# Optimization experiments

Hardware: AMD Instinct MI355X
Metric: run time of the kernel (lower is better)

Reference implementation:

```python
import jax, jax.numpy as jnp
import numpy as np

N_NODES = 50000
N_EDGES = 320000
B = 4096          # subgraph batch: users/items/subg nodes
IN_N = 64         # in_nfeats
IN_E = 16         # in_efeats
OUT_E = 2 * IN_E  # out_edge_feats = in_efeats*2
H = 4             # num_heads
D = 64            # latent dim per layer (latent_dim=[64,64])
L = 2             # num EGAT layers


def setup_inputs() -> dict:
    key = jax.random.key(0)
    ks = iter(jax.random.split(key, 48))
    def nrm(shape, s=0.05):
        return jax.random.normal(next(ks), shape, dtype=jnp.float32) * s
    inp = {}
    inp['x'] = jax.random.normal(next(ks), (N_NODES, IN_N), dtype=jnp.float32)
    inp['efeat'] = jax.random.normal(next(ks), (N_EDGES, IN_E), dtype=jnp.float32)
    inp['efeat2'] = jax.random.normal(next(ks), (N_EDGES, IN_N), dtype=jnp.float32)
    inp['edge_mask'] = (jax.random.uniform(next(ks), (N_EDGES,)) > 0.1).astype(jnp.float32)
    inp['edge_mask2'] = (jax.random.uniform(next(ks), (N_EDGES,)) > 0.1).astype(jnp.float32)
    inp['src'] = jax.random.randint(next(ks), (N_EDGES,), 0, N_NODES, dtype=jnp.int32)
    inp['dst'] = jax.random.randint(next(ks), (N_EDGES,), 0, N_NODES, dtype=jnp.int32)
    inp['user_idx'] = jnp.arange(0, B, dtype=jnp.int32)          # ntype==0
    inp['item_idx'] = jnp.arange(B, 2 * B, dtype=jnp.int32)      # ntype==1
    inp['subg_idx'] = jnp.arange(2 * B, 3 * B, dtype=jnp.int32)  # ntype==-1
    # stacked per-layer EGAT params (layer dims identical since IN_N == D)
    inp['loc_wni'] = nrm((L, D, H * OUT_E))
    inp['loc_wnj'] = nrm((L, D, H * OUT_E))
    inp['loc_we'] = nrm((L, IN_E, H * OUT_E))
    inp['loc_attn'] = nrm((L, H, OUT_E))
    inp['loc_wnode'] = nrm((L, D, H * D))
    inp['agg1_w'] = nrm((L, H * D, D))
    inp['agg1_b'] = jnp.zeros((L, D), jnp.float32)
    inp['glob_wni'] = nrm((L, D, H * OUT_E))
    inp['glob_wnj'] = nrm((L, D, H * OUT_E))
    inp['glob_we'] = nrm((L, IN_N, H * OUT_E))
    inp['glob_attn'] = nrm((L, H, OUT_E))
    inp['glob_wnode'] = nrm((L, D, H * D))
    inp['agg2_w'] = nrm((L, H * D, D))
    inp['agg2_b'] = jnp.zeros((L, D), jnp.float32)
    inp['w1_ui'] = nrm((2 * L * D, 128))
    inp['b1_ui'] = jnp.zeros((128,), jnp.float32)
    inp['w1_sg'] = nrm((L * D, 128))
    inp['b1_sg'] = jnp.zeros((128,), jnp.float32)
    inp['w2_ui'] = nrm((128, 1))
    inp['b2_ui'] = jnp.zeros((1,), jnp.float32)
    inp['w2_sg'] = nrm((128, 1))
    inp['b2_sg'] = jnp.zeros((1,), jnp.float32)
    return inp


def _egat(x, e, norm, src, dst, wni, wnj, we, attn, wnode):
    # edge feature: f_ij = LeakyReLU(W_ni x_i + W_nj x_j + W_e e_ij), slope 0.2 (DGL EGATConv)
    f = (x @ wni)[src] + (x @ wnj)[dst] + e @ we            # (E, H*OUT_E)
    f = jax.nn.leaky_relu(f.reshape(-1, H, OUT_E), 0.2)
    scores = jnp.einsum('ehd,hd->eh', f, attn)              # (E, H)
    # edge softmax over incoming edges of each dst node
    m = jax.ops.segment_max(scores, dst, num_segments=N_NODES)
    m = jnp.where(jnp.isfinite(m), m, 0.0)
    ex = jnp.exp(scores - m[dst])
    denom = jax.ops.segment_sum(ex, dst, num_segments=N_NODES)
    a = ex / (denom[dst] + 1e-9)
    a = a * norm[:, None]                                    # per-edge norm (edge mask) weighting
    fn = (x @ wnode).reshape(-1, H, D)                       # (N, H, D)
    msg = fn[src] * a[:, :, None]                            # (E, H, D)
    out = jax.ops.segment_sum(msg, dst, num_segments=N_NODES)
    return out, a


def reference(x, efeat, efeat2, edge_mask, edge_mask2, src, dst, user_idx, item_idx, subg_idx,
              loc_wni, loc_wnj, loc_we, loc_attn, loc_wnode, agg1_w, agg1_b,
              glob_wni, glob_wnj, glob_we, glob_attn, glob_wnode, agg2_w, agg2_b,
              w1_ui, b1_ui, w1_sg, b1_sg, w2_ui, b2_ui, w2_sg, b2_sg):
    h = x
    ui_states, sg_states = [], []
    for l in range(L):
        out, _ = _egat(h, efeat, edge_mask, src, dst,
                       loc_wni[l], loc_wnj[l], loc_we[l], loc_attn[l], loc_wnode[l])
        h = jax.nn.elu(out.reshape(N_NODES, H * D) @ agg1_w[l] + agg1_b[l])
        ui_states.append(h)
        out, _ = _egat(h, efeat2, edge_mask2, src, dst,
                       glob_wni[l], glob_wnj[l], glob_we[l], glob_attn[l], glob_wnode[l])
        h = jax.nn.leaky_relu(out.reshape(N_NODES, H * D) @ agg2_w[l] + agg2_b[l], 0.01)
        sg_states.append(h)
    ui = jnp.concatenate(ui_states, axis=1)   # (N, L*D)
    sg = jnp.concatenate(sg_states, axis=1)   # (N, L*D)
    ui_x = jnp.concatenate([ui[user_idx], ui[item_idx]], axis=1)  # (B, 2*L*D)
    sg_x = sg[subg_idx]                                           # (B, L*D)
    ui_h = jax.nn.relu(ui_x @ w1_ui + b1_ui)  # dropout is identity in eval
    sg_h = jax.nn.relu(sg_x @ w1_sg + b1_sg)
    ui_out = jax.nn.sigmoid(ui_h @ w2_ui + b2_ui)[:, 0]
    sg_out = jax.nn.sigmoid(sg_h @ w2_sg + b2_sg)[:, 0]
    return (sg_out, ui_out)
```

## Files before the change

kernel.cpp:

```cpp
#include <hip/hip_runtime.h>
#include <math.h>

#define NN 50000
#define NE 320000
#define BATCH 4096

typedef __bf16 bf16x8 __attribute__((ext_vector_type(8)));
typedef float floatx4 __attribute__((ext_vector_type(4)));
typedef unsigned short ushort;
typedef unsigned int uint;

__device__ __forceinline__ float lrelu02(float x) { return x > 0.f ? x : 0.2f * x; }
__device__ __forceinline__ float b2f(ushort h) { return __uint_as_float(((uint)h) << 16); }
__device__ __forceinline__ float b2f_lo(uint u) { return __uint_as_float(u << 16); }
__device__ __forceinline__ float b2f_hi(uint u) { return __uint_as_float(u & 0xffff0000u); }
__device__ __forceinline__ ushort f2b(float x) {
    uint u = __float_as_uint(x);
    return (ushort)((u + 0x7fffu + ((u >> 16) & 1u)) >> 16);
}

template <int GLOB>
__global__ __launch_bounds__(256) void score_frag(
    const float* __restrict__ ef,
    const ushort* __restrict__ Bfrag,
    const ushort* __restrict__ hb,
    const int* __restrict__ eidx, const int* __restrict__ srcv,
    const int* __restrict__ dstv,
    const float* __restrict__ attn, float* __restrict__ scv)
{
    constexpr int KTOT = GLOB ? 192 : 160;
    constexpr int NR = KTOT / 32;
    constexpr int EFR = GLOB ? 2 : 1;
    constexpr int LDA = GLOB ? 64 : 16;
    __shared__ __align__(16) ushort As[128 * KTOT];
    const int tid = threadIdx.x;
    const int w = tid >> 6, lane = tid & 63;
    const int quad = lane >> 4, l16 = lane & 15;
    const int row = (blockIdx.x << 6) + 16 * w + l16;

    const int e_o = eidx[row];
    const int s_n = srcv[row];
    const int d_n = dstv[row];

    bf16x8 bfr[NR];
#pragma unroll
    for (int rnd = 0; rnd < EFR; rnd++) {
        uint4 av = make_uint4(0u, 0u, 0u, 0u);
        int k0 = rnd * 32 + quad * 8;
        if (GLOB || quad < 2) {
            const float* ap = ef + (size_t)e_o * LDA + k0;
            float4 f0 = *(const float4*)ap;
            float4 f1 = *(const float4*)(ap + 4);
            av.x = (uint)f2b(f0.x) | ((uint)f2b(f0.y) << 16);
            av.y = (uint)f2b(f0.z) | ((uint)f2b(f0.w) << 16);
            av.z = (uint)f2b(f1.x) | ((uint)f2b(f1.y) << 16);
            av.w = (uint)f2b(f1.z) | ((uint)f2b(f1.w) << 16);
        }
        *(uint4*)&bfr[rnd] = av;
    }
#pragma unroll
    for (int rr = 0; rr < 2; rr++)
        bfr[EFR + rr] = *(const bf16x8*)(hb + (size_t)s_n * 64 + rr * 32 + quad * 8);
#pragma unroll
    for (int rr = 0; rr < 2; rr++)
        bfr[EFR + 2 + rr] = *(const bf16x8*)(hb + (size_t)d_n * 64 + rr * 32 + quad * 8);

    for (int i = tid; i < 128 * KTOT / 8; i += 256)
        *(uint4*)(As + (size_t)i * 8) = *(const uint4*)(Bfrag + (size_t)i * 8);
    __syncthreads();

    floatx4 acc[8];
#pragma unroll
    for (int c = 0; c < 8; c++)
#pragma unroll
        for (int r = 0; r < 4; r++) acc[c][r] = 0.f;

#pragma unroll
    for (int rnd = 0; rnd < NR; rnd++) {
#pragma unroll
        for (int c = 0; c < 8; c++) {
            bf16x8 afr = *(const bf16x8*)(As + ((size_t)(c * NR + rnd) * 64 + lane) * 8);
            acc[c] = __builtin_amdgcn_mfma_f32_16x16x32_bf16(afr, bfr[rnd], acc[c], 0, 0, 0);
        }
    }

    float ph[4] = {0.f, 0.f, 0.f, 0.f};
#pragma unroll
    for (int c = 0; c < 8; c++) {
        int fbase = 16 * c + quad * 4;
        float4 at4 = *(const float4*)(attn + fbase);
        float v = lrelu02(acc[c][0]) * at4.x;
        v = fmaf(lrelu02(acc[c][1]), at4.y, v);
        v = fmaf(lrelu02(acc[c][2]), at4.z, v);
        v = fmaf(lrelu02(acc[c][3]), at4.w, v);
        ph[fbase >> 5] += v;
    }
#pragma unroll
    for (int h = 0; h < 4; h++) {
        ph[h] += __shfl_xor(ph[h], 16);
        ph[h] += __shfl_xor(ph[h], 32);
    }
    if (quad == 0)
        *(float4*)(scv + (size_t)row * 4) = make_float4(ph[0], ph[1], ph[2], ph[3]);
}

__global__ __launch_bounds__(256) void gemm_agg(
    const ushort* __restrict__ A, int M,
    const ushort* __restrict__ Bt,
    const float* __restrict__ bias, int act,
    ushort* __restrict__ outb)
{
    __shared__ __align__(16) ushort As[64 * 32];
    __shared__ __align__(16) ushort Bs[64 * 32];
    const int tid = threadIdx.x;
    const int row0 = blockIdx.x << 6;
    const int w = tid >> 6, lane = tid & 63;
    const int quad = lane >> 4, l16 = lane & 15;
    const int arow = tid >> 2, c0 = (tid & 3) << 3;
    const int agrow = row0 + arow;

    floatx4 acc[4];
#pragma unroll
    for (int c = 0; c < 4; c++)
#pragma unroll
        for (int r = 0; r < 4; r++) acc[c][r] = 0.f;

    for (int kt = 0; kt < 256; kt += 32) {
        uint4 av = make_uint4(0u, 0u, 0u, 0u);
        if (agrow < M)
            av = *(const uint4*)(A + (size_t)agrow * 256 + kt + c0);
        *(uint4*)(As + arow * 32 + c0) = av;
        {
            int bn = tid >> 2, bk = (tid & 3) << 3;
            *(uint4*)(Bs + bn * 32 + bk) = *(const uint4*)(Bt + (size_t)bn * 256 + kt + bk);
        }
        __syncthreads();
        bf16x8 af = *(const bf16x8*)(As + (16 * w + l16) * 32 + quad * 8);
#pragma unroll
        for (int c = 0; c < 4; c++) {
            bf16x8 bfv = *(const bf16x8*)(Bs + (16 * c + l16) * 32 + quad * 8);
            acc[c] = __builtin_amdgcn_mfma_f32_16x16x32_bf16(af, bfv, acc[c], 0, 0, 0);
        }
        if (kt + 32 < 256) __syncthreads();
    }
#pragma unroll
    for (int r = 0; r < 4; r++) {
        int gr = row0 + 16 * w + quad * 4 + r;
        if (gr < M) {
#pragma unroll
            for (int c = 0; c < 4; c++) {
                int col = 16 * c + l16;
                float v = acc[c][r] + bias[col];
                if (act == 0) v = v > 0.f ? v : (__expf(v) - 1.f);
                else          v = v > 0.f ? v : 0.01f * v;
                outb[(size_t)gr * 64 + col] = f2b(v);
            }
        }
    }
}

__global__ void k_count(const int* __restrict__ dst, int* __restrict__ deg, int E)
{
    for (int i = blockIdx.x * blockDim.x + threadIdx.x; i < E; i += gridDim.x * blockDim.x)
        atomicAdd(&deg[dst[i]], 1);
}

__global__ __launch_bounds__(256) void scan_local(
    const int* __restrict__ deg, int* __restrict__ rowptr, int* __restrict__ partials, int N)
{
    __shared__ int sd[256];
    int tid = threadIdx.x;
    int i = blockIdx.x * 256 + tid;
    int v = (i < N) ? deg[i] : 0;
    sd[tid] = v; __syncthreads();
#pragma unroll
    for (int off = 1; off < 256; off <<= 1) {
        int t = (tid >= off) ? sd[tid - off] : 0;
        __syncthreads();
        sd[tid] += t;
        __syncthreads();
    }
    if (i < N) rowptr[i] = sd[tid] - v;
    if (tid == 255) partials[blockIdx.x] = sd[255];
}

__global__ __launch_bounds__(256) void scan_partials(int* __restrict__ partials, int nb)
{
    __shared__ int sd[256];
    int tid = threadIdx.x;
    int v = (tid < nb) ? partials[tid] : 0;
    sd[tid] = v; __syncthreads();
#pragma unroll
    for (int off = 1; off < 256; off <<= 1) {
        int t = (tid >= off) ? sd[tid - off] : 0;
        __syncthreads();
        sd[tid] += t;
        __syncthreads();
    }
    if (tid < nb) partials[tid] = sd[tid] - v;
}

__global__ void scan_add(int* __restrict__ rowptr, const int* __restrict__ partials, int N, int E)
{
    int i = blockIdx.x * 256 + threadIdx.x;
    if (i < N) rowptr[i] += partials[i >> 8];
    if (i == 0) rowptr[N] = E;
}

__global__ void k_scatter(const int* __restrict__ dst, const int* __restrict__ rowptr,
                          int* __restrict__ cnt, int* __restrict__ eidx, int E)
{
    for (int i = blockIdx.x * blockDim.x + threadIdx.x; i < E; i += gridDim.x * blockDim.x) {
        int d = dst[i];
        int p = rowptr[d] + atomicAdd(&cnt[d], 1);
        eidx[p] = i;
    }
}

__global__ void k_sort_buckets(const int* __restrict__ rowptr, int* __restrict__ eidx, int N)
{
    int n = blockIdx.x * blockDim.x + threadIdx.x;
    if (n >= N) return;
    int beg = rowptr[n], end = rowptr[n + 1];
    for (int i = beg + 1; i < end; i++) {
        int v = eidx[i];
        int j = i - 1;
        while (j >= beg && eidx[j] > v) { eidx[j + 1] = eidx[j]; j--; }
        eidx[j + 1] = v;
    }
}

__global__ void k_emit_perm(const int* __restrict__ eidx, const int* __restrict__ src,
                            const int* __restrict__ dst,
                            const float* __restrict__ m1, const float* __restrict__ m2,
                            int* __restrict__ srcp, int* __restrict__ dstp,
                            float* __restrict__ m1p, float* __restrict__ m2p, int E)
{
    int p = blockIdx.x * blockDim.x + threadIdx.x;
    if (p < E) {
        int e = eidx[p];
        srcp[p] = src[e];
        dstp[p] = dst[e];
        m1p[p] = m1[e];
        m2p[p] = m2[e];
    }
}

__global__ void k_cvt(const float* __restrict__ in, ushort* __restrict__ out, int n)
{
    for (int i = blockIdx.x * blockDim.x + threadIdx.x; i < n; i += gridDim.x * blockDim.x)
        out[i] = f2b(in[i]);
}

__global__ void k_prep_score_all(const float* __restrict__ loc_we, const float* __restrict__ glob_we,
                                 const float* __restrict__ loc_wni, const float* __restrict__ glob_wni,
                                 const float* __restrict__ loc_wnj, const float* __restrict__ glob_wnj,
                                 ushort* __restrict__ B)
{
    int idx = blockIdx.x * 256 + threadIdx.x;
    if (idx >= 4 * 24576) return;
    int e = idx / 24576, rem = idx % 24576;
    int layer = e >> 1, gl = e & 1;
    int KTOT = gl ? 192 : 160;
    int NR = KTOT / 32;
    int ef_end = gl ? 64 : 32;
    int ef_real = gl ? 64 : 16;
    if (rem >= 128 * KTOT) return;
    int j = rem & 7, lane = (rem >> 3) & 63, t = rem >> 9;
    int c = t / NR, rnd = t % NR;
    int m = 16 * c + (lane & 15);
    int k = 32 * rnd + (lane >> 4) * 8 + j;
    const float* we  = (gl ? glob_we  + layer * 64 * 128 : loc_we  + layer * 16 * 128);
    const float* wni = (gl ? glob_wni : loc_wni) + layer * 64 * 128;
    const float* wnj = (gl ? glob_wnj : loc_wnj) + layer * 64 * 128;
    float v;
    if (k < ef_end)            v = (k < ef_real) ? we[k * 128 + m] : 0.f;
    else if (k < ef_end + 64)  v = wni[(k - ef_end) * 128 + m];
    else                       v = wnj[(k - ef_end - 64) * 128 + m];
    B[e * 24576 + rem] = f2b(v);
}

__global__ void k_fold_all(const float* __restrict__ loc_wnode, const float* __restrict__ agg1_w,
                           const float* __restrict__ glob_wnode, const float* __restrict__ agg2_w,
                           ushort* __restrict__ B)
{
    int e = blockIdx.x >> 6;
    int idx = (blockIdx.x & 63) * 256 + threadIdx.x;
    int layer = e >> 1, gl = e & 1;
    const float* wnode = (gl ? glob_wnode : loc_wnode) + layer * 64 * 256;
    const float* aggw  = (gl ? agg2_w : agg1_w) + layer * 256 * 64;
    int j = idx >> 8, col = idx & 255;
    int h = col >> 6, ii = col & 63;
    float s = 0.f;
#pragma unroll 8
    for (int k = 0; k < 64; k++)
        s = fmaf(wnode[ii * 256 + h * 64 + k], aggw[(h * 64 + k) * 64 + j], s);
    B[e * 16384 + j * 256 + col] = f2b(s);
}

__global__ __launch_bounds__(256) void node_fused(
    const float* __restrict__ scv,
    const int* __restrict__ rowptr, const int* __restrict__ srcp,
    const float* __restrict__ maskp,
    const ushort* __restrict__ hsrc,
    ushort* __restrict__ zb)
{
    int tid = threadIdx.x;
    int n = (blockIdx.x << 4) | (tid >> 4);
    int sl = tid & 15;
    int beg = rowptr[n], end = rowptr[n + 1];
    float l0 = 0.f, l1 = 0.f, l2 = 0.f, l3 = 0.f;
    float acc[4][4] = {};
#pragma unroll 2
    for (int i = beg; i < end; i++) {
        float4 s4 = *(const float4*)(scv + (size_t)i * 4);
        float mk = maskp[i];
        int s = srcp[i];
        uint2 hvv = *(const uint2*)(hsrc + (size_t)s * 64 + sl * 4);
        float t0 = __expf(s4.x), t1 = __expf(s4.y), t2 = __expf(s4.z), t3 = __expf(s4.w);
        l0 += t0; l1 += t1; l2 += t2; l3 += t3;
        float a0 = t0 * mk, a1 = t1 * mk, a2 = t2 * mk, a3 = t3 * mk;
        float hv[4] = { b2f_lo(hvv.x), b2f_hi(hvv.x), b2f_lo(hvv.y), b2f_hi(hvv.y) };
#pragma unroll
        for (int c = 0; c < 4; c++) {
            acc[0][c] = fmaf(a0, hv[c], acc[0][c]);
            acc[1][c] = fmaf(a1, hv[c], acc[1][c]);
            acc[2][c] = fmaf(a2, hv[c], acc[2][c]);
            acc[3][c] = fmaf(a3, hv[c], acc[3][c]);
        }
    }
    float inv[4] = { 1.f / (l0 + 1e-9f), 1.f / (l1 + 1e-9f),
                     1.f / (l2 + 1e-9f), 1.f / (l3 + 1e-9f) };
#pragma unroll
    for (int h = 0; h < 4; h++) {
        uint2 o;
        o.x = (uint)f2b(acc[h][0] * inv[h]) | ((uint)f2b(acc[h][1] * inv[h]) << 16);
        o.y = (uint)f2b(acc[h][2] * inv[h]) | ((uint)f2b(acc[h][3] * inv[h]) << 16);
        *(uint2*)(zb + (size_t)n * 256 + h * 64 + sl * 4) = o;
    }
}

__global__ __launch_bounds__(256) void final_ui(
    const ushort* __restrict__ s0, const ushort* __restrict__ s1,
    const int* __restrict__ uidx, const int* __restrict__ iidx,
    const float* __restrict__ w1, const float* __restrict__ b1,
    const float* __restrict__ w2, const float* __restrict__ b2, float* __restrict__ out)
{
    __shared__ float xs[4][256];
    int tid = threadIdx.x, wid = tid >> 6, lane = tid & 63;
    int r = (blockIdx.x << 2) + wid;
    int u = uidx[r], it = iidx[r];
    xs[wid][lane]       = b2f(s0[(size_t)u * 64 + lane]);
    xs[wid][64 + lane]  = b2f(s1[(size_t)u * 64 + lane]);
    xs[wid][128 + lane] = b2f(s0[(size_t)it * 64 + lane]);
    xs[wid][192 + lane] = b2f(s1[(size_t)it * 64 + lane]);
    __syncthreads();
    int c = lane << 1;
    float a0 = b1[c], a1 = b1[c + 1];
    for (int k = 0; k < 256; k++) {
        float xv = xs[wid][k];
        float2 wv = *(const float2*)(w1 + (size_t)k * 128 + c);
        a0 = fmaf(xv, wv.x, a0);
        a1 = fmaf(xv, wv.y, a1);
    }
    a0 = fmaxf(a0, 0.f);
    a1 = fmaxf(a1, 0.f);
    float2 w2v = *(const float2*)(w2 + c);
    float p = a0 * w2v.x + a1 * w2v.y;
#pragma unroll
    for (int mm = 1; mm < 64; mm <<= 1) p += __shfl_xor(p, mm);
    if (lane == 0) out[r] = 1.f / (1.f + __expf(-(p + b2[0])));
}

__global__ __launch_bounds__(256) void final_sg(
    const ushort* __restrict__ s0, const ushort* __restrict__ s1,
    const int* __restrict__ gidx,
    const float* __restrict__ w1, const float* __restrict__ b1,
    const float* __restrict__ w2, const float* __restrict__ b2, float* __restrict__ out)
{
    __shared__ float xs[4][128];
    int tid = threadIdx.x, wid = tid >> 6, lane = tid & 63;
    int r = (blockIdx.x << 2) + wid;
    int n = gidx[r];
    xs[wid][lane]      = b2f(s0[(size_t)n * 64 + lane]);
    xs[wid][64 + lane] = b2f(s1[(size_t)n * 64 + lane]);
    __syncthreads();
    int c = lane << 1;
    float a0 = b1[c], a1 = b1[c + 1];
    for (int k = 0; k < 128; k++) {
        float xv = xs[wid][k];
        float2 wv = *(const float2*)(w1 + (size_t)k * 128 + c);
        a0 = fmaf(xv, wv.x, a0);
        a1 = fmaf(xv, wv.y, a1);
    }
    a0 = fmaxf(a0, 0.f);
    a1 = fmaxf(a1, 0.f);
    float2 w2v = *(const float2*)(w2 + c);
    float p = a0 * w2v.x + a1 * w2v.y;
#pragma unroll
    for (int mm = 1; mm < 64; mm <<= 1) p += __shfl_xor(p, mm);
    if (lane == 0) out[r] = 1.f / (1.f + __expf(-(p + b2[0])));
}

extern "C" void kernel_launch(void* const* d_in, const int* in_sizes, int n_in,
                              void* d_out, int out_size, void* d_ws, size_t ws_size,
                              hipStream_t stream)
{
    const float* x       = (const float*)d_in[0];
    const float* efeat   = (const float*)d_in[1];
    const float* efeat2  = (const float*)d_in[2];
    const float* mask1   = (const float*)d_in[3];
    const float* mask2   = (const float*)d_in[4];
    const int*   src     = (const int*)d_in[5];
    const int*   dst     = (const int*)d_in[6];
    const int*   uidx    = (const int*)d_in[7];
    const int*   iidx    = (const int*)d_in[8];
    const int*   gidx    = (const int*)d_in[9];
    const float* loc_wni = (const float*)d_in[10];
    const float* loc_wnj = (const float*)d_in[11];
    const float* loc_we  = (const float*)d_in[12];
    const float* loc_attn= (const float*)d_in[13];
    const float* loc_wnode=(const float*)d_in[14];
    const float* agg1_w  = (const float*)d_in[15];
    const float* agg1_b  = (const float*)d_in[16];
    const float* glob_wni= (const float*)d_in[17];
    const float* glob_wnj= (const float*)d_in[18];
    const float* glob_we = (const float*)d_in[19];
    const float* glob_attn=(const float*)d_in[20];
    const float* glob_wnode=(const float*)d_in[21];
    const float* agg2_w  = (const float*)d_in[22];
    const float* agg2_b  = (const float*)d_in[23];
    const float* w1_ui   = (const float*)d_in[24];
    const float* b1_ui   = (const float*)d_in[25];
    const float* w1_sg   = (const float*)d_in[26];
    const float* b1_sg   = (const float*)d_in[27];
    const float* w2_ui   = (const float*)d_in[28];
    const float* b2_ui   = (const float*)d_in[29];
    const float* w2_sg   = (const float*)d_in[30];
    const float* b2_sg   = (const float*)d_in[31];

    char* wsp = (char*)d_ws;
    auto carve = [&](size_t bytes) { char* p = wsp; wsp += (bytes + 255) & ~(size_t)255; return p; };
    ushort* zb    = (ushort*)carve((size_t)NN * 256 * 2);
    ushort* hb[5];
    for (int i = 0; i < 5; i++) hb[i] = (ushort*)carve((size_t)NN * 64 * 2);
    float*  scv   = (float*)carve((size_t)NE * 16);
    float*  m1p   = (float*)carve((size_t)NE * 4);
    float*  m2p   = (float*)carve((size_t)NE * 4);
    int*    srcp  = (int*)carve((size_t)NE * 4);
    int*    dstp  = (int*)carve((size_t)NE * 4);
    int*    eidx  = (int*)carve((size_t)NE * 4);
    ushort* Bsc   = (ushort*)carve(4 * 24576 * 2);
    ushort* Bfold = (ushort*)carve(4 * 16384 * 2);
    int* deg      = (int*)carve(NN * 4);
    int* rowptr   = (int*)carve((NN + 4) * 4);
    int* partials = (int*)carve(256 * 4);

    k_prep_score_all<<<384, 256, 0, stream>>>(loc_we, glob_we, loc_wni, glob_wni,
                                              loc_wnj, glob_wnj, Bsc);
    k_fold_all<<<256, 256, 0, stream>>>(loc_wnode, agg1_w, glob_wnode, agg2_w, Bfold);
    hipMemsetAsync(deg, 0, NN * sizeof(int), stream);
    k_count<<<1280, 256, 0, stream>>>(dst, deg, NE);
    scan_local<<<196, 256, 0, stream>>>(deg, rowptr, partials, NN);
    scan_partials<<<1, 256, 0, stream>>>(partials, 196);
    scan_add<<<196, 256, 0, stream>>>(rowptr, partials, NN, NE);
    hipMemsetAsync(deg, 0, NN * sizeof(int), stream);
    k_scatter<<<1280, 256, 0, stream>>>(dst, rowptr, deg, eidx, NE);
    k_sort_buckets<<<196, 256, 0, stream>>>(rowptr, eidx, NN);
    k_emit_perm<<<1250, 256, 0, stream>>>(eidx, src, dst, mask1, mask2,
                                          srcp, dstp, m1p, m2p, NE);
    k_cvt<<<3200, 256, 0, stream>>>(x, hb[0], NN * 64);

    auto egat = [&](const ushort* hin, int e, const float* maskp, const float* attn,
                    const float* aggb, int act, ushort* hout) {
        int is_glob = e & 1;
        if (is_glob)
            score_frag<1><<<5000, 256, 0, stream>>>(efeat2, Bsc + e * 24576, hin,
                                                    eidx, srcp, dstp, attn, scv);
        else
            score_frag<0><<<5000, 256, 0, stream>>>(efeat, Bsc + e * 24576, hin,
                                                    eidx, srcp, dstp, attn, scv);
        node_fused<<<NN / 16, 256, 0, stream>>>(scv, rowptr, srcp, maskp, hin, zb);
        gemm_agg<<<782, 256, 0, stream>>>(zb, NN, Bfold + e * 16384, aggb, act, hout);
    };

    egat(hb[0], 0, m1p, loc_attn,        agg1_b,      0, hb[1]);
    egat(hb[1], 1, m2p, glob_attn,       agg2_b,      1, hb[2]);
    egat(hb[2], 2, m1p, loc_attn + 128,  agg1_b + 64, 0, hb[3]);
    egat(hb[3], 3, m2p, glob_attn + 128, agg2_b + 64, 1, hb[4]);

    float* out = (float*)d_out;
    final_sg<<<BATCH / 4, 256, 0, stream>>>(hb[2], hb[4], gidx, w1_sg, b1_sg, w2_sg, b2_sg, out);
    final_ui<<<BATCH / 4, 256, 0, stream>>>(hb[1], hb[3], uidx, iidx, w1_ui, b1_ui, w2_ui, b2_ui, out + BATCH);
}
```

Before: 598.9 us.

## Pre-permute edge features to bf16 and make score kernel persistent with prefetch

```diff
diff --git a/kernel.cpp b/kernel.cpp
--- a/kernel.cpp
+++ b/kernel.cpp
@@ -18,90 +18,109 @@
     uint u = __float_as_uint(x);
     return (ushort)((u + 0x7fffu + ((u >> 16) & 1u)) >> 16);
 }
+__device__ __forceinline__ uint pk2(float a, float b) {
+    return (uint)f2b(a) | ((uint)f2b(b) << 16);
+}
 
 template <int GLOB>
-__global__ __launch_bounds__(256) void score_frag(
-    const float* __restrict__ ef,
+__global__ __launch_bounds__(256, 3) void score_frag(
+    const ushort* __restrict__ efp,
     const ushort* __restrict__ Bfrag,
     const ushort* __restrict__ hb,
-    const int* __restrict__ eidx, const int* __restrict__ srcv,
-    const int* __restrict__ dstv,
+    const int* __restrict__ srcv, const int* __restrict__ dstv,
     const float* __restrict__ attn, float* __restrict__ scv)
 {
     constexpr int KTOT = GLOB ? 192 : 160;
     constexpr int NR = KTOT / 32;
     constexpr int EFR = GLOB ? 2 : 1;
-    constexpr int LDA = GLOB ? 64 : 16;
     __shared__ __align__(16) ushort As[128 * KTOT];
     const int tid = threadIdx.x;
     const int w = tid >> 6, lane = tid & 63;
     const int quad = lane >> 4, l16 = lane & 15;
-    const int row = (blockIdx.x << 6) + 16 * w + l16;
-
-    const int e_o = eidx[row];
-    const int s_n = srcv[row];
-    const int d_n = dstv[row];
-
-    bf16x8 bfr[NR];
-#pragma unroll
-    for (int rnd = 0; rnd < EFR; rnd++) {
-        uint4 av = make_uint4(0u, 0u, 0u, 0u);
-        int k0 = rnd * 32 + quad * 8;
-        if (GLOB || quad < 2) {
-            const float* ap = ef + (size_t)e_o * LDA + k0;
-            float4 f0 = *(const float4*)ap;
-            float4 f1 = *(const float4*)(ap + 4);
-            av.x = (uint)f2b(f0.x) | ((uint)f2b(f0.y) << 16);
-            av.y = (uint)f2b(f0.z) | ((uint)f2b(f0.w) << 16);
-            av.z = (uint)f2b(f1.x) | ((uint)f2b(f1.y) << 16);
-            av.w = (uint)f2b(f1.z) | ((uint)f2b(f1.w) << 16);
-        }
-        *(uint4*)&bfr[rnd] = av;
-    }
-#pragma unroll
-    for (int rr = 0; rr < 2; rr++)
-        bfr[EFR + rr] = *(const bf16x8*)(hb + (size_t)s_n * 64 + rr * 32 + quad * 8);
-#pragma unroll
-    for (int rr = 0; rr < 2; rr++)
-        bfr[EFR + 2 + rr] = *(const bf16x8*)(hb + (size_t)d_n * 64 + rr * 32 + quad * 8);
 
     for (int i = tid; i < 128 * KTOT / 8; i += 256)
         *(uint4*)(As + (size_t)i * 8) = *(const uint4*)(Bfrag + (size_t)i * 8);
+
+    auto loadB = [&](bf16x8* dstf, int r, int s, int d) {
+        if (GLOB) {
+#pragma unroll
+            for (int rr = 0; rr < 2; rr++)
+                dstf[rr] = *(const bf16x8*)(efp + (size_t)r * 64 + rr * 32 + quad * 8);
+        } else {
+            bf16x8 v;
+            *(uint4*)&v = make_uint4(0u, 0u, 0u, 0u);
+            if (quad < 2) v = *(const bf16x8*)(efp + (size_t)r * 16 + quad * 8);
+            dstf[0] = v;
+        }
+#pragma unroll
+        for (int rr = 0; rr < 2; rr++)
+            dstf[EFR + rr] = *(const bf16x8*)(hb + (size_t)s * 64 + rr * 32 + quad * 8);
+#pragma unroll
+        for (int rr = 0; rr < 2; rr++)
+            dstf[EFR + 2 + rr] = *(const bf16x8*)(hb + (size_t)d * 64 + rr * 32 + quad * 8);
+    };
+
+    const int lstep = gridDim.x << 6;
+    int row = (blockIdx.x << 6) + 16 * w + l16;
+    bf16x8 bfr[NR];
+    {
+        int s0 = srcv[row], d0 = dstv[row];
+        loadB(bfr, row, s0, d0);
+    }
+    int row1 = row + lstep;
+    int sn1 = 0, dn1 = 0;
+    if (row1 < NE) { sn1 = srcv[row1]; dn1 = dstv[row1]; }
+
+    float4 at4[8];
+#pragma unroll
+    for (int c = 0; c < 8; c++) at4[c] = *(const float4*)(attn + 16 * c + quad * 4);
+
     __syncthreads();
 
-    floatx4 acc[8];
-#pragma unroll
-    for (int c = 0; c < 8; c++)
-#pragma unroll
-        for (int r = 0; r < 4; r++) acc[c][r] = 0.f;
-
-#pragma unroll
-    for (int rnd = 0; rnd < NR; rnd++) {
+    while (true) {
+        const bool more = (row1 < NE);
+        int row2 = row1 + lstep;
+        int sn2 = 0, dn2 = 0;
+        if (row2 < NE) { sn2 = srcv[row2]; dn2 = dstv[row2]; }
+        bf16x8 nbfr[NR];
+        if (more) loadB(nbfr, row1, sn1, dn1);
+
+        floatx4 acc[8];
+#pragma unroll
+        for (int c = 0; c < 8; c++)
+#pragma unroll
+            for (int r = 0; r < 4; r++) acc[c][r] = 0.f;
+
+#pragma unroll
+        for (int rnd = 0; rnd < NR; rnd++)
+#pragma unroll
+            for (int c = 0; c < 8; c++) {
+                bf16x8 afr = *(const bf16x8*)(As + ((size_t)(c * NR + rnd) * 64 + lane) * 8);
+                acc[c] = __builtin_amdgcn_mfma_f32_16x16x32_bf16(afr, bfr[rnd], acc[c], 0, 0, 0);
+            }
+
+        float ph[4] = {0.f, 0.f, 0.f, 0.f};
 #pragma unroll
         for (int c = 0; c < 8; c++) {
-            bf16x8 afr = *(const bf16x8*)(As + ((size_t)(c * NR + rnd) * 64 + lane) * 8);
-            acc[c] = __builtin_amdgcn_mfma_f32_16x16x32_bf16(afr, bfr[rnd], acc[c], 0, 0, 0);
-        }
-    }
-
-    float ph[4] = {0.f, 0.f, 0.f, 0.f};
-#pragma unroll
-    for (int c = 0; c < 8; c++) {
-        int fbase = 16 * c + quad * 4;
-        float4 at4 = *(const float4*)(attn + fbase);
-        float v = lrelu02(acc[c][0]) * at4.x;
-        v = fmaf(lrelu02(acc[c][1]), at4.y, v);
-        v = fmaf(lrelu02(acc[c][2]), at4.z, v);
-        v = fmaf(lrelu02(acc[c][3]), at4.w, v);
-        ph[fbase >> 5] += v;
-    }
-#pragma unroll
-    for (int h = 0; h < 4; h++) {
-        ph[h] += __shfl_xor(ph[h], 16);
-        ph[h] += __shfl_xor(ph[h], 32);
-    }
-    if (quad == 0)
-        *(float4*)(scv + (size_t)row * 4) = make_float4(ph[0], ph[1], ph[2], ph[3]);
+            float v = lrelu02(acc[c][0]) * at4[c].x;
+            v = fmaf(lrelu02(acc[c][1]), at4[c].y, v);
+            v = fmaf(lrelu02(acc[c][2]), at4[c].z, v);
+            v = fmaf(lrelu02(acc[c][3]), at4[c].w, v);
+            ph[c >> 1] += v;
+        }
+#pragma unroll
+        for (int h = 0; h < 4; h++) {
+            ph[h] += __shfl_xor(ph[h], 16);
+            ph[h] += __shfl_xor(ph[h], 32);
+        }
+        if (quad == 0)
+            *(float4*)(scv + (size_t)row * 4) = make_float4(ph[0], ph[1], ph[2], ph[3]);
+
+        if (!more) break;
+        row = row1; row1 = row2; sn1 = sn2; dn1 = dn2;
+#pragma unroll
+        for (int r = 0; r < NR; r++) bfr[r] = nbfr[r];
+    }
 }
 
 __global__ __launch_bounds__(256) void gemm_agg(
@@ -233,16 +252,40 @@
 __global__ void k_emit_perm(const int* __restrict__ eidx, const int* __restrict__ src,
                             const int* __restrict__ dst,
                             const float* __restrict__ m1, const float* __restrict__ m2,
+                            const float* __restrict__ ef, const float* __restrict__ ef2,
                             int* __restrict__ srcp, int* __restrict__ dstp,
-                            float* __restrict__ m1p, float* __restrict__ m2p, int E)
-{
-    int p = blockIdx.x * blockDim.x + threadIdx.x;
-    if (p < E) {
-        int e = eidx[p];
+                            float* __restrict__ m1p, float* __restrict__ m2p,
+                            ushort* __restrict__ efp_l, ushort* __restrict__ efp_g, int E)
+{
+    int t = blockIdx.x * blockDim.x + threadIdx.x;
+    if (t >= 4 * E) return;
+    int p = t >> 2, part = t & 3;
+    int e = eidx[p];
+    {
+        const float4* s4 = (const float4*)(ef2 + (size_t)e * 64 + part * 16);
+        float4 f0 = s4[0], f1 = s4[1], f2v = s4[2], f3 = s4[3];
+        uint4 o0, o1;
+        o0.x = pk2(f0.x, f0.y);  o0.y = pk2(f0.z, f0.w);
+        o0.z = pk2(f1.x, f1.y);  o0.w = pk2(f1.z, f1.w);
+        o1.x = pk2(f2v.x, f2v.y); o1.y = pk2(f2v.z, f2v.w);
+        o1.z = pk2(f3.x, f3.y);  o1.w = pk2(f3.z, f3.w);
+        uint4* dp = (uint4*)(efp_g + (size_t)p * 64 + part * 16);
+        dp[0] = o0; dp[1] = o1;
+    }
+    if (part == 0) {
         srcp[p] = src[e];
         dstp[p] = dst[e];
         m1p[p] = m1[e];
         m2p[p] = m2[e];
+        const float4* s4 = (const float4*)(ef + (size_t)e * 16);
+        float4 f0 = s4[0], f1 = s4[1], f2v = s4[2], f3 = s4[3];
+        uint4 o0, o1;
+        o0.x = pk2(f0.x, f0.y);  o0.y = pk2(f0.z, f0.w);
+        o0.z = pk2(f1.x, f1.y);  o0.w = pk2(f1.z, f1.w);
+        o1.x = pk2(f2v.x, f2v.y); o1.y = pk2(f2v.z, f2v.w);
+        o1.z = pk2(f3.x, f3.y);  o1.w = pk2(f3.z, f3.w);
+        uint4* dp = (uint4*)(efp_l + (size_t)p * 16);
+        dp[0] = o0; dp[1] = o1;
     }
 }
 
@@ -450,6 +493,8 @@
     int*    srcp  = (int*)carve((size_t)NE * 4);
     int*    dstp  = (int*)carve((size_t)NE * 4);
     int*    eidx  = (int*)carve((size_t)NE * 4);
+    ushort* efp_l = (ushort*)carve((size_t)NE * 16 * 2);
+    ushort* efp_g = (ushort*)carve((size_t)NE * 64 * 2);
     ushort* Bsc   = (ushort*)carve(4 * 24576 * 2);
     ushort* Bfold = (ushort*)carve(4 * 16384 * 2);
     int* deg      = (int*)carve(NN * 4);
@@ -467,19 +512,19 @@
     hipMemsetAsync(deg, 0, NN * sizeof(int), stream);
     k_scatter<<<1280, 256, 0, stream>>>(dst, rowptr, deg, eidx, NE);
     k_sort_buckets<<<196, 256, 0, stream>>>(rowptr, eidx, NN);
-    k_emit_perm<<<1250, 256, 0, stream>>>(eidx, src, dst, mask1, mask2,
-                                          srcp, dstp, m1p, m2p, NE);
+    k_emit_perm<<<5000, 256, 0, stream>>>(eidx, src, dst, mask1, mask2, efeat, efeat2,
+                                          srcp, dstp, m1p, m2p, efp_l, efp_g, NE);
     k_cvt<<<3200, 256, 0, stream>>>(x, hb[0], NN * 64);
 
     auto egat = [&](const ushort* hin, int e, const float* maskp, const float* attn,
                     const float* aggb, int act, ushort* hout) {
         int is_glob = e & 1;
         if (is_glob)
-            score_frag<1><<<5000, 256, 0, stream>>>(efeat2, Bsc + e * 24576, hin,
-                                                    eidx, srcp, dstp, attn, scv);
+            score_frag<1><<<1024, 256, 0, stream>>>(efp_g, Bsc + e * 24576, hin,
+                                                    srcp, dstp, attn, scv);
         else
-            score_frag<0><<<5000, 256, 0, stream>>>(efeat, Bsc + e * 24576, hin,
-                                                    eidx, srcp, dstp, attn, scv);
+            score_frag<0><<<1024, 256, 0, stream>>>(efp_l, Bsc + e * 24576, hin,
+                                                    srcp, dstp, attn, scv);
         node_fused<<<NN / 16, 256, 0, stream>>>(scv, rowptr, srcp, maskp, hin, zb);
         gemm_agg<<<782, 256, 0, stream>>>(zb, NN, Bfold + e * 16384, aggb, act, hout);
     };
```

Result: slower. 1.101 ms (+83.8%).

## Read edges in original order in score kernel and scatter scores via inverse permutation

Applied to the files above, without the earlier changes.

```diff
diff --git a/kernel.cpp b/kernel.cpp
--- a/kernel.cpp
+++ b/kernel.cpp
@@ -18,14 +18,17 @@
     uint u = __float_as_uint(x);
     return (ushort)((u + 0x7fffu + ((u >> 16) & 1u)) >> 16);
 }
+__device__ __forceinline__ uint pk2(float a, float b) {
+    return (uint)f2b(a) | ((uint)f2b(b) << 16);
+}
 
 template <int GLOB>
-__global__ __launch_bounds__(256) void score_frag(
+__global__ __launch_bounds__(512, 6) void score_frag(
     const float* __restrict__ ef,
     const ushort* __restrict__ Bfrag,
     const ushort* __restrict__ hb,
-    const int* __restrict__ eidx, const int* __restrict__ srcv,
-    const int* __restrict__ dstv,
+    const int* __restrict__ srcv, const int* __restrict__ dstv,
+    const int* __restrict__ pos,
     const float* __restrict__ attn, float* __restrict__ scv)
 {
     constexpr int KTOT = GLOB ? 192 : 160;
@@ -36,11 +39,11 @@
     const int tid = threadIdx.x;
     const int w = tid >> 6, lane = tid & 63;
     const int quad = lane >> 4, l16 = lane & 15;
-    const int row = (blockIdx.x << 6) + 16 * w + l16;
-
-    const int e_o = eidx[row];
+    const int row = (blockIdx.x << 7) + 16 * w + l16;
+
     const int s_n = srcv[row];
     const int d_n = dstv[row];
+    const int prow = pos[row];
 
     bf16x8 bfr[NR];
 #pragma unroll
@@ -48,13 +51,13 @@
         uint4 av = make_uint4(0u, 0u, 0u, 0u);
         int k0 = rnd * 32 + quad * 8;
         if (GLOB || quad < 2) {
-            const float* ap = ef + (size_t)e_o * LDA + k0;
+            const float* ap = ef + (size_t)row * LDA + k0;
             float4 f0 = *(const float4*)ap;
             float4 f1 = *(const float4*)(ap + 4);
-            av.x = (uint)f2b(f0.x) | ((uint)f2b(f0.y) << 16);
-            av.y = (uint)f2b(f0.z) | ((uint)f2b(f0.w) << 16);
-            av.z = (uint)f2b(f1.x) | ((uint)f2b(f1.y) << 16);
-            av.w = (uint)f2b(f1.z) | ((uint)f2b(f1.w) << 16);
+            av.x = pk2(f0.x, f0.y);
+            av.y = pk2(f0.z, f0.w);
+            av.z = pk2(f1.x, f1.y);
+            av.w = pk2(f1.z, f1.w);
         }
         *(uint4*)&bfr[rnd] = av;
     }
@@ -65,7 +68,7 @@
     for (int rr = 0; rr < 2; rr++)
         bfr[EFR + 2 + rr] = *(const bf16x8*)(hb + (size_t)d_n * 64 + rr * 32 + quad * 8);
 
-    for (int i = tid; i < 128 * KTOT / 8; i += 256)
+    for (int i = tid; i < 128 * KTOT / 8; i += 512)
         *(uint4*)(As + (size_t)i * 8) = *(const uint4*)(Bfrag + (size_t)i * 8);
     __syncthreads();
 
@@ -101,7 +104,7 @@
         ph[h] += __shfl_xor(ph[h], 32);
     }
     if (quad == 0)
-        *(float4*)(scv + (size_t)row * 4) = make_float4(ph[0], ph[1], ph[2], ph[3]);
+        *(float4*)(scv + (size_t)prow * 4) = make_float4(ph[0], ph[1], ph[2], ph[3]);
 }
 
 __global__ __launch_bounds__(256) void gemm_agg(
@@ -230,19 +233,18 @@
     }
 }
 
-__global__ void k_emit_perm(const int* __restrict__ eidx, const int* __restrict__ src,
-                            const int* __restrict__ dst,
-                            const float* __restrict__ m1, const float* __restrict__ m2,
-                            int* __restrict__ srcp, int* __restrict__ dstp,
-                            float* __restrict__ m1p, float* __restrict__ m2p, int E)
+__global__ void k_perm_small(const int* __restrict__ eidx, const int* __restrict__ src,
+                             const float* __restrict__ m1, const float* __restrict__ m2,
+                             int* __restrict__ srcp, float* __restrict__ m1p,
+                             float* __restrict__ m2p, int* __restrict__ pos, int E)
 {
     int p = blockIdx.x * blockDim.x + threadIdx.x;
     if (p < E) {
         int e = eidx[p];
         srcp[p] = src[e];
-        dstp[p] = dst[e];
         m1p[p] = m1[e];
         m2p[p] = m2[e];
+        pos[e] = p;
     }
 }
 
@@ -448,7 +450,7 @@
     float*  m1p   = (float*)carve((size_t)NE * 4);
     float*  m2p   = (float*)carve((size_t)NE * 4);
     int*    srcp  = (int*)carve((size_t)NE * 4);
-    int*    dstp  = (int*)carve((size_t)NE * 4);
+    int*    pos   = (int*)carve((size_t)NE * 4);
     int*    eidx  = (int*)carve((size_t)NE * 4);
     ushort* Bsc   = (ushort*)carve(4 * 24576 * 2);
     ushort* Bfold = (ushort*)carve(4 * 16384 * 2);
@@ -467,19 +469,19 @@
     hipMemsetAsync(deg, 0, NN * sizeof(int), stream);
     k_scatter<<<1280, 256, 0, stream>>>(dst, rowptr, deg, eidx, NE);
     k_sort_buckets<<<196, 256, 0, stream>>>(rowptr, eidx, NN);
-    k_emit_perm<<<1250, 256, 0, stream>>>(eidx, src, dst, mask1, mask2,
-                                          srcp, dstp, m1p, m2p, NE);
+    k_perm_small<<<1250, 256, 0, stream>>>(eidx, src, mask1, mask2,
+                                           srcp, m1p, m2p, pos, NE);
     k_cvt<<<3200, 256, 0, stream>>>(x, hb[0], NN * 64);
 
     auto egat = [&](const ushort* hin, int e, const float* maskp, const float* attn,
                     const float* aggb, int act, ushort* hout) {
         int is_glob = e & 1;
         if (is_glob)
-            score_frag<1><<<5000, 256, 0, stream>>>(efeat2, Bsc + e * 24576, hin,
-                                                    eidx, srcp, dstp, attn, scv);
+            score_frag<1><<<2500, 512, 0, stream>>>(efeat2, Bsc + e * 24576, hin,
+                                                    src, dst, pos, attn, scv);
         else
-            score_frag<0><<<5000, 256, 0, stream>>>(efeat, Bsc + e * 24576, hin,
-                                                    eidx, srcp, dstp, attn, scv);
+            score_frag<0><<<2500, 512, 0, stream>>>(efeat, Bsc + e * 24576, hin,
+                                                    src, dst, pos, attn, scv);
         node_fused<<<NN / 16, 256, 0, stream>>>(scv, rowptr, srcp, maskp, hin, zb);
         gemm_agg<<<782, 256, 0, stream>>>(zb, NN, Bfold + e * 16384, aggb, act, hout);
     };
```

Result: no change. 588.6 us (-1.7%).
